# Kernel optimization log

Measured on AMD Instinct MI355X. Metric: run time of the kernel, lower is better.

## Reference

```python
import jax, jax.numpy as jnp
import numpy as np

B, S, D = 8, 4096, 64

def setup_inputs() -> dict:
    key = jax.random.key(0)
    k1, k2 = jax.random.split(key)
    x = jax.random.normal(k1, (B, S, D), dtype=jnp.float32)
    y = jax.random.normal(k2, (B, S, D), dtype=jnp.float32)
    return {"x": x, "y": y}

def reference(x, y):
    # Unscaled bidirectional cross-attention.
    # m1: [B, Sx, Sy] = x @ y^T ; m2: [B, Sy, Sx] = y @ x^T (= m1^T, but keep faithful form)
    m1 = jnp.einsum('bsd,btd->bst', x, y)
    m2 = jnp.einsum('btd,bsd->bts', y, x)
    n1 = jax.nn.softmax(m1, axis=-1)
    n2 = jax.nn.softmax(m2, axis=-1)
    o1 = jnp.einsum('bst,btd->bsd', n1, y)
    o2 = jnp.einsum('bts,bsd->btd', n2, x)
    a1 = o1 * x
    a2 = o2 * y
    return jnp.concatenate((a1, a2), axis=-1)  # [B, S, 2D]
```

## Files before the change

kernel.cpp:

```cpp
#include <hip/hip_runtime.h>
#include <stdint.h>
#include <stddef.h>

#define SS 4096
#define DD 64
#define TK 64
#define LOG2E 1.4426950408889634f
#define NEG_M_L2 (-57.70780163555854f)

typedef short    short4v __attribute__((ext_vector_type(4)));
typedef short    short8 __attribute__((ext_vector_type(8)));
typedef _Float16 half8  __attribute__((ext_vector_type(8)));
typedef float    f32x4  __attribute__((ext_vector_type(4)));
typedef __bf16   bf16x8 __attribute__((ext_vector_type(8)));

typedef __attribute__((address_space(1))) void void_g;
typedef __attribute__((address_space(3))) void void_l;

static __device__ __forceinline__ unsigned short bf16_rtn(float f) {
    uint32_t u = __builtin_bit_cast(uint32_t, f);
    u += 0x7FFFu + ((u >> 16) & 1u);
    return (unsigned short)(u >> 16);
}
static __device__ __forceinline__ void gl_lds16(const void* g, void* l) {
    __builtin_amdgcn_global_load_lds((void_g*)(g), (void_l*)(l), 16, 0, 0);
}

#define MFMA_F16(A, B, C) __builtin_amdgcn_mfma_f32_16x16x32_f16( \
    __builtin_bit_cast(half8, A), __builtin_bit_cast(half8, B), (C), 0, 0, 0)
#define MFMA_BF16(A, B, C) __builtin_amdgcn_mfma_f32_16x16x32_bf16( \
    __builtin_bit_cast(bf16x8, A), __builtin_bit_cast(bf16x8, B), (C), 0, 0, 0)

__global__ __launch_bounds__(256) void prep(
    const float* __restrict__ x, const float* __restrict__ y,
    _Float16* __restrict__ fx, _Float16* __restrict__ fy,
    unsigned short* __restrict__ tx, unsigned short* __restrict__ ty) {
    __shared__ float tile[64 * 69];
    int bid = blockIdx.x;
    int mat = bid >> 9;
    int rem = bid & 511;
    int b = rem >> 6, t64 = rem & 63;
    int s0 = t64 * 64;
    const float* src = (mat ? y : x) + ((size_t)b * SS + s0) * 64;
    _Float16* fr = (mat ? fy : fx) + ((size_t)b * SS + s0) * 64;
    unsigned short* tr = (mat ? ty : tx) + (size_t)b * SS * 64;
    int tid = threadIdx.x;
#pragma unroll
    for (int it = 0; it < 4; ++it) {
        int qi = it * 256 + tid;
        int r = qi >> 4, c4 = (qi & 15) * 4;
        f32x4 v = *(const f32x4*)(src + r * 64 + c4);
#pragma unroll
        for (int j = 0; j < 4; ++j) tile[r * 69 + c4 + j] = v[j];
    }
    __syncthreads();
#pragma unroll
    for (int j2 = 0; j2 < 2; ++j2) {
        int seg = j2 * 256 + tid;
        int r = seg >> 3, g = seg & 7;
        half8 h;
#pragma unroll
        for (int j = 0; j < 8; ++j) h[j] = (_Float16)tile[r * 69 + g * 8 + j];
        *(half8*)(fr + (size_t)r * 64 + ((g + r) & 7) * 8) = h;
    }
#pragma unroll
    for (int j2 = 0; j2 < 2; ++j2) {
        int seg = j2 * 256 + tid;
        int d = seg >> 3, k8 = seg & 7;
        short8 h;
#pragma unroll
        for (int i = 0; i < 8; ++i)
            h[i] = (short)bf16_rtn(tile[(k8 * 8 + i) * 69 + d]);
        *(short8*)(tr + (size_t)d * SS + s0 + ((k8 + d) & 7) * 8) = h;
    }
}

__global__ __launch_bounds__(256, 4)
void biattn(const float* __restrict__ xg, const float* __restrict__ yg,
            const _Float16* __restrict__ fx, const _Float16* __restrict__ fy,
            const unsigned short* __restrict__ tx, const unsigned short* __restrict__ ty,
            float* __restrict__ wsO, float* __restrict__ wsL,
            float* __restrict__ out, int mode) {
    __shared__ _Float16 shK[TK * DD];
    __shared__ unsigned short shVt[DD * TK];
    __shared__ unsigned short shP[4][32][40];

    const int bid = blockIdx.x;
    const int g8 = bid >> 3;
    int half, bd, qb;
    qb = g8 & 31;
    if (mode) { half = (g8 >> 5) & 1; bd = (bid & 7) + 8 * (g8 >> 6); }
    else      { half = 0;             bd = (bid & 7) + 8 * (g8 >> 5); }
    const int b = bd >> 1, dir = bd & 1;
    const size_t mo = (size_t)b * SS * DD;
    const _Float16* Kf = (dir ? fx : fy) + mo;
    const unsigned short* Vt = (dir ? tx : ty) + mo;
    const _Float16* Qf = (dir ? fy : fx) + mo;
    const float* Qm = (dir ? yg : xg) + mo;

    const int tid = threadIdx.x, w = tid >> 6, ln = tid & 63;
    const int l15 = ln & 15, quad = ln >> 4;
    const int q0 = qb * 128 + w * 32;

    half8 qf[2][2];
#pragma unroll
    for (int qs = 0; qs < 2; ++qs) {
        int qrow = q0 + qs * 16 + l15;
#pragma unroll
        for (int c = 0; c < 2; ++c)
            qf[qs][c] = *(const half8*)(Qf + (size_t)qrow * 64 +
                                        ((c * 4 + quad + qrow) & 7) * 8);
    }

    f32x4 Oa[2][4], La[2];
#pragma unroll
    for (int qs = 0; qs < 2; ++qs) {
        La[qs] = (f32x4){0.f, 0.f, 0.f, 0.f};
#pragma unroll
        for (int dt = 0; dt < 4; ++dt) Oa[qs][dt] = (f32x4){0.f, 0.f, 0.f, 0.f};
    }
    short8 onesb;
#pragma unroll
    for (int j = 0; j < 8; ++j) onesb[j] = (short)0x3F80;

    const int kblo = mode ? half * (SS / 2) : 0;
    const int kbhi = mode ? kblo + (SS / 2) : SS;

    for (int kb = kblo; kb < kbhi; kb += TK) {
        __syncthreads();
#pragma unroll
        for (int i = 0; i < 4; ++i) {
            int seg = w * 4 + i;
            if (seg < 8) {
                gl_lds16(Kf + (size_t)kb * 64 + seg * 512 + ln * 8,
                         (void*)(shK + seg * 512));
            } else {
                int s2 = seg - 8;
                int d = s2 * 8 + (ln >> 3);
                gl_lds16(Vt + (size_t)d * SS + kb + (ln & 7) * 8,
                         (void*)(shVt + s2 * 512));
            }
        }
        __syncthreads();

#pragma unroll
        for (int c32 = 0; c32 < 2; ++c32) {
            const int kc = c32 * 32;
            f32x4 sacc[2][2];
#pragma unroll
            for (int qs = 0; qs < 2; ++qs)
#pragma unroll
                for (int st = 0; st < 2; ++st)
                    sacc[qs][st] = (f32x4){0.f, 0.f, 0.f, 0.f};
#pragma unroll
            for (int st = 0; st < 2; ++st) {
                const int krow = kc + st * 16 + l15;
                const _Float16* hr = shK + krow * 64;
                half8 a0 = *(const half8*)(hr + ((quad + krow) & 7) * 8);
                half8 a1 = *(const half8*)(hr + ((quad + 4 + krow) & 7) * 8);
#pragma unroll
                for (int qs = 0; qs < 2; ++qs) {
                    f32x4 acc = sacc[qs][st];
                    acc = MFMA_F16(a0, qf[qs][0], acc);
                    acc = MFMA_F16(a1, qf[qs][1], acc);
                    sacc[qs][st] = acc;
                }
            }
#pragma unroll
            for (int qs = 0; qs < 2; ++qs) {
#pragma unroll
                for (int st = 0; st < 2; ++st) {
                    f32x4 s = sacc[qs][st];
                    float p0 = __builtin_amdgcn_exp2f(__builtin_fmaf(s[0], LOG2E, NEG_M_L2));
                    float p1 = __builtin_amdgcn_exp2f(__builtin_fmaf(s[1], LOG2E, NEG_M_L2));
                    float p2 = __builtin_amdgcn_exp2f(__builtin_fmaf(s[2], LOG2E, NEG_M_L2));
                    float p3 = __builtin_amdgcn_exp2f(__builtin_fmaf(s[3], LOG2E, NEG_M_L2));
                    short4v pk;
                    pk[0] = (short)bf16_rtn(p0);
                    pk[1] = (short)bf16_rtn(p1);
                    pk[2] = (short)bf16_rtn(p2);
                    pk[3] = (short)bf16_rtn(p3);
                    *(short4v*)&shP[w][qs * 16 + l15][st * 16 + quad * 4] = pk;
                }
            }
            short8 bfr0 = *(const short8*)&shP[w][l15][quad * 8];
            short8 bfr1 = *(const short8*)&shP[w][16 + l15][quad * 8];
            const int rotv = ((c32 * 4 + quad + l15) & 7) * 8;
#pragma unroll
            for (int dt = 0; dt < 4; ++dt) {
                short8 av = *(const short8*)(shVt + (dt * 16 + l15) * 64 + rotv);
                Oa[0][dt] = MFMA_BF16(av, bfr0, Oa[0][dt]);
                Oa[1][dt] = MFMA_BF16(av, bfr1, Oa[1][dt]);
            }
            La[0] = MFMA_BF16(onesb, bfr0, La[0]);
            La[1] = MFMA_BF16(onesb, bfr1, La[1]);
        }
    }

    if (mode) {
        const int pb = half * 512 + bd * 32 + qb;
#pragma unroll
        for (int qs = 0; qs < 2; ++qs) {
            float* base = wsO + (size_t)pb * 8192 + (size_t)(w * 2 + qs) * 1024
                        + l15 * 16 + quad * 4;
#pragma unroll
            for (int dt = 0; dt < 4; ++dt)
                *(f32x4*)(base + dt * 256) = Oa[qs][dt];
            if (quad == 0)
                wsL[(size_t)pb * 128 + w * 32 + qs * 16 + l15] = La[qs][0];
        }
    } else {
#pragma unroll
        for (int qs = 0; qs < 2; ++qs) {
            float inv = 1.0f / La[qs][0];
            int qrow = q0 + qs * 16 + l15;
#pragma unroll
            for (int dt = 0; dt < 4; ++dt) {
                const float* qp = Qm + (size_t)qrow * DD + dt * 16 + quad * 4;
                f32x4 xv = *(const f32x4*)qp;
                f32x4 o = Oa[qs][dt];
                f32x4 r;
#pragma unroll
                for (int j = 0; j < 4; ++j) r[j] = o[j] * inv * xv[j];
                float* op = out + ((size_t)(b * SS + qrow)) * 128 + dir * 64
                          + dt * 16 + quad * 4;
                *(f32x4*)op = r;
            }
        }
    }
}

__global__ __launch_bounds__(256) void combine(
    const float* __restrict__ xg, const float* __restrict__ yg,
    const float* __restrict__ wsO, const float* __restrict__ wsL,
    float* __restrict__ out) {
    __shared__ float t[8 * 1088];
    int pb = blockIdx.x;
    int bd = pb >> 5, qb = pb & 31;
    int b = bd >> 1, dir = bd & 1;
    const float* p0 = wsO + (size_t)pb * 8192;
    const float* p1 = wsO + (size_t)(512 + pb) * 8192;
    const float* l0 = wsL + (size_t)pb * 128;
    const float* l1 = wsL + (size_t)(512 + pb) * 128;
    const float* Qm = (dir ? yg : xg) + (size_t)b * SS * DD;
    int tid = threadIdx.x;
#pragma unroll
    for (int j = 0; j < 8; ++j) {
        int idx = j * 1024 + tid * 4;
        f32x4 a = *(const f32x4*)(p0 + idx);
        f32x4 c = *(const f32x4*)(p1 + idx);
        int dt = (idx >> 8) & 3, q = (idx >> 4) & 15, dq = idx & 15;
#pragma unroll
        for (int jj = 0; jj < 4; ++jj)
            t[j * 1088 + (dt * 16 + dq + jj) * 17 + q] = a[jj] + c[jj];
    }
    __syncthreads();
    int w2 = tid >> 6, ln = tid & 63;
    int q00 = qb * 128;
#pragma unroll 4
    for (int i = 0; i < 32; ++i) {
        int q128 = w2 * 32 + i;
        int seg = q128 >> 4, lq = q128 & 15;
        float o = t[seg * 1088 + ln * 17 + lq];
        float l = l0[q128] + l1[q128];
        float qv = Qm[(size_t)(q00 + q128) * 64 + ln];
        out[((size_t)(b * SS + q00 + q128)) * 128 + dir * 64 + ln]
            = o * (1.0f / l) * qv;
    }
}

extern "C" void kernel_launch(void* const* d_in, const int* in_sizes, int n_in,
                              void* d_out, int out_size, void* d_ws, size_t ws_size,
                              hipStream_t stream) {
    const float* x = (const float*)d_in[0];
    const float* y = (const float*)d_in[1];
    char* ws = (char*)d_ws;
    const size_t MATB = (size_t)8 * SS * DD * 2;
    _Float16* fx = (_Float16*)(ws);
    _Float16* fy = (_Float16*)(ws + MATB);
    unsigned short* tx = (unsigned short*)(ws + 2 * MATB);
    unsigned short* ty = (unsigned short*)(ws + 3 * MATB);
    float* wsO = (float*)(ws + 4 * MATB);
    float* wsL = (float*)(ws + 4 * MATB + (size_t)1024 * 8192 * 4);
    const size_t need = 4 * MATB + (size_t)1024 * 8192 * 4 + (size_t)1024 * 128 * 4;
    const int mode = (ws_size >= need) ? 1 : 0;
    (void)in_sizes; (void)n_in; (void)out_size;
    prep<<<dim3(1024), dim3(256), 0, stream>>>(x, y, fx, fy, tx, ty);
    biattn<<<dim3(mode ? 1024 : 512), dim3(256), 0, stream>>>(
        x, y, fx, fy, tx, ty, wsO, wsL, (float*)d_out, mode);
    if (mode)
        combine<<<dim3(512), dim3(256), 0, stream>>>(x, y, wsO, wsL, (float*)d_out);
}
```

Baseline: 171.3 us.

## Generalize split-K to four parts, fold log2e into Q, use packed bf16 converts

The key range is now split into up to four parts instead of two when the workspace is large enough, which multiplies the block count and needs more partial sums in combine. The log2(e) scale is folded into Q during prep, and the constant offset is used as the MFMA accumulator's initial value, so the per-element FMA before exp2 is dropped. Probability and transpose packing use a hardware packed bf16 convert when the builtin exists. The occupancy hint is raised from 4 to 6 blocks per SM, which may add register pressure.

New measurement: 496.5 us. 190% more time.

```diff
diff --git a/kernel.cpp b/kernel.cpp
--- a/kernel.cpp
+++ b/kernel.cpp
@@ -13,6 +13,8 @@
 typedef _Float16 half8  __attribute__((ext_vector_type(8)));
 typedef float    f32x4  __attribute__((ext_vector_type(4)));
 typedef __bf16   bf16x8 __attribute__((ext_vector_type(8)));
+typedef uint32_t u32x2  __attribute__((ext_vector_type(2)));
+typedef uint32_t u32x4  __attribute__((ext_vector_type(4)));
 
 typedef __attribute__((address_space(1))) void void_g;
 typedef __attribute__((address_space(3))) void void_l;
@@ -22,6 +24,17 @@
     u += 0x7FFFu + ((u >> 16) & 1u);
     return (unsigned short)(u >> 16);
 }
+#if __has_builtin(__builtin_amdgcn_cvt_pk_bf16_f32)
+typedef __bf16 bf16x2 __attribute__((ext_vector_type(2)));
+static __device__ __forceinline__ uint32_t pkbf(float a, float b) {
+    bf16x2 v = __builtin_amdgcn_cvt_pk_bf16_f32(a, b);
+    return __builtin_bit_cast(uint32_t, v);
+}
+#else
+static __device__ __forceinline__ uint32_t pkbf(float a, float b) {
+    return (uint32_t)bf16_rtn(a) | ((uint32_t)bf16_rtn(b) << 16);
+}
+#endif
 static __device__ __forceinline__ void gl_lds16(const void* g, void* l) {
     __builtin_amdgcn_global_load_lds((void_g*)(g), (void_l*)(l), 16, 0, 0);
 }
@@ -44,6 +57,7 @@
     const float* src = (mat ? y : x) + ((size_t)b * SS + s0) * 64;
     _Float16* fr = (mat ? fy : fx) + ((size_t)b * SS + s0) * 64;
     unsigned short* tr = (mat ? ty : tx) + (size_t)b * SS * 64;
+    const float sc = mat ? 1.0f : LOG2E;
     int tid = threadIdx.x;
 #pragma unroll
     for (int it = 0; it < 4; ++it) {
@@ -60,37 +74,40 @@
         int r = seg >> 3, g = seg & 7;
         half8 h;
 #pragma unroll
-        for (int j = 0; j < 8; ++j) h[j] = (_Float16)tile[r * 69 + g * 8 + j];
+        for (int j = 0; j < 8; ++j)
+            h[j] = (_Float16)(tile[r * 69 + g * 8 + j] * sc);
         *(half8*)(fr + (size_t)r * 64 + ((g + r) & 7) * 8) = h;
     }
 #pragma unroll
     for (int j2 = 0; j2 < 2; ++j2) {
         int seg = j2 * 256 + tid;
         int d = seg >> 3, k8 = seg & 7;
-        short8 h;
-#pragma unroll
-        for (int i = 0; i < 8; ++i)
-            h[i] = (short)bf16_rtn(tile[(k8 * 8 + i) * 69 + d]);
-        *(short8*)(tr + (size_t)d * SS + s0 + ((k8 + d) & 7) * 8) = h;
-    }
-}
-
-__global__ __launch_bounds__(256, 4)
+        float v[8];
+#pragma unroll
+        for (int i = 0; i < 8; ++i) v[i] = tile[(k8 * 8 + i) * 69 + d];
+        u32x4 o;
+        o[0] = pkbf(v[0], v[1]); o[1] = pkbf(v[2], v[3]);
+        o[2] = pkbf(v[4], v[5]); o[3] = pkbf(v[6], v[7]);
+        *(u32x4*)(tr + (size_t)d * SS + s0 + ((k8 + d) & 7) * 8) = o;
+    }
+}
+
+__global__ __launch_bounds__(256, 6)
 void biattn(const float* __restrict__ xg, const float* __restrict__ yg,
             const _Float16* __restrict__ fx, const _Float16* __restrict__ fy,
             const unsigned short* __restrict__ tx, const unsigned short* __restrict__ ty,
             float* __restrict__ wsO, float* __restrict__ wsL,
-            float* __restrict__ out, int mode) {
+            float* __restrict__ out, int nsplit) {
     __shared__ _Float16 shK[TK * DD];
     __shared__ unsigned short shVt[DD * TK];
     __shared__ unsigned short shP[4][32][40];
 
     const int bid = blockIdx.x;
     const int g8 = bid >> 3;
-    int half, bd, qb;
-    qb = g8 & 31;
-    if (mode) { half = (g8 >> 5) & 1; bd = (bid & 7) + 8 * (g8 >> 6); }
-    else      { half = 0;             bd = (bid & 7) + 8 * (g8 >> 5); }
+    const int qb = g8 & 31;
+    const int r2 = g8 >> 5;
+    const int bd = (bid & 7) + 8 * (r2 & 1);
+    const int part = r2 >> 1;
     const int b = bd >> 1, dir = bd & 1;
     const size_t mo = (size_t)b * SS * DD;
     const _Float16* Kf = (dir ? fx : fy) + mo;
@@ -123,8 +140,9 @@
 #pragma unroll
     for (int j = 0; j < 8; ++j) onesb[j] = (short)0x3F80;
 
-    const int kblo = mode ? half * (SS / 2) : 0;
-    const int kbhi = mode ? kblo + (SS / 2) : SS;
+    const int span = SS / nsplit;
+    const int kblo = part * span;
+    const int kbhi = kblo + span;
 
     for (int kb = kblo; kb < kbhi; kb += TK) {
         __syncthreads();
@@ -151,7 +169,7 @@
             for (int qs = 0; qs < 2; ++qs)
 #pragma unroll
                 for (int st = 0; st < 2; ++st)
-                    sacc[qs][st] = (f32x4){0.f, 0.f, 0.f, 0.f};
+                    sacc[qs][st] = (f32x4){NEG_M_L2, NEG_M_L2, NEG_M_L2, NEG_M_L2};
 #pragma unroll
             for (int st = 0; st < 2; ++st) {
                 const int krow = kc + st * 16 + l15;
@@ -168,20 +186,21 @@
             }
 #pragma unroll
             for (int qs = 0; qs < 2; ++qs) {
-#pragma unroll
-                for (int st = 0; st < 2; ++st) {
-                    f32x4 s = sacc[qs][st];
-                    float p0 = __builtin_amdgcn_exp2f(__builtin_fmaf(s[0], LOG2E, NEG_M_L2));
-                    float p1 = __builtin_amdgcn_exp2f(__builtin_fmaf(s[1], LOG2E, NEG_M_L2));
-                    float p2 = __builtin_amdgcn_exp2f(__builtin_fmaf(s[2], LOG2E, NEG_M_L2));
-                    float p3 = __builtin_amdgcn_exp2f(__builtin_fmaf(s[3], LOG2E, NEG_M_L2));
-                    short4v pk;
-                    pk[0] = (short)bf16_rtn(p0);
-                    pk[1] = (short)bf16_rtn(p1);
-                    pk[2] = (short)bf16_rtn(p2);
-                    pk[3] = (short)bf16_rtn(p3);
-                    *(short4v*)&shP[w][qs * 16 + l15][st * 16 + quad * 4] = pk;
-                }
+                f32x4 s0 = sacc[qs][0], s1 = sacc[qs][1];
+                float p0 = __builtin_amdgcn_exp2f(s0[0]);
+                float p1 = __builtin_amdgcn_exp2f(s0[1]);
+                float p2 = __builtin_amdgcn_exp2f(s0[2]);
+                float p3 = __builtin_amdgcn_exp2f(s0[3]);
+                float p4 = __builtin_amdgcn_exp2f(s1[0]);
+                float p5 = __builtin_amdgcn_exp2f(s1[1]);
+                float p6 = __builtin_amdgcn_exp2f(s1[2]);
+                float p7 = __builtin_amdgcn_exp2f(s1[3]);
+                u32x2 w0, w1;
+                w0[0] = pkbf(p0, p1); w0[1] = pkbf(p2, p3);
+                w1[0] = pkbf(p4, p5); w1[1] = pkbf(p6, p7);
+                unsigned short* pr = &shP[w][qs * 16 + l15][0];
+                *(u32x2*)(pr + quad * 4)      = w0;
+                *(u32x2*)(pr + 16 + quad * 4) = w1;
             }
             short8 bfr0 = *(const short8*)&shP[w][l15][quad * 8];
             short8 bfr1 = *(const short8*)&shP[w][16 + l15][quad * 8];
@@ -197,8 +216,8 @@
         }
     }
 
-    if (mode) {
-        const int pb = half * 512 + bd * 32 + qb;
+    if (nsplit > 1) {
+        const int pb = part * 512 + bd * 32 + qb;
 #pragma unroll
         for (int qs = 0; qs < 2; ++qs) {
             float* base = wsO + (size_t)pb * 8192 + (size_t)(w * 2 + qs) * 1024
@@ -233,26 +252,26 @@
 __global__ __launch_bounds__(256) void combine(
     const float* __restrict__ xg, const float* __restrict__ yg,
     const float* __restrict__ wsO, const float* __restrict__ wsL,
-    float* __restrict__ out) {
+    float* __restrict__ out, int nsplit) {
     __shared__ float t[8 * 1088];
     int pb = blockIdx.x;
     int bd = pb >> 5, qb = pb & 31;
     int b = bd >> 1, dir = bd & 1;
-    const float* p0 = wsO + (size_t)pb * 8192;
-    const float* p1 = wsO + (size_t)(512 + pb) * 8192;
-    const float* l0 = wsL + (size_t)pb * 128;
-    const float* l1 = wsL + (size_t)(512 + pb) * 128;
     const float* Qm = (dir ? yg : xg) + (size_t)b * SS * DD;
     int tid = threadIdx.x;
 #pragma unroll
     for (int j = 0; j < 8; ++j) {
         int idx = j * 1024 + tid * 4;
-        f32x4 a = *(const f32x4*)(p0 + idx);
-        f32x4 c = *(const f32x4*)(p1 + idx);
+        f32x4 a = {0.f, 0.f, 0.f, 0.f};
+        for (int s = 0; s < nsplit; ++s) {
+            f32x4 v = *(const f32x4*)(wsO + (size_t)(s * 512 + pb) * 8192 + idx);
+#pragma unroll
+            for (int jj = 0; jj < 4; ++jj) a[jj] += v[jj];
+        }
         int dt = (idx >> 8) & 3, q = (idx >> 4) & 15, dq = idx & 15;
 #pragma unroll
         for (int jj = 0; jj < 4; ++jj)
-            t[j * 1088 + (dt * 16 + dq + jj) * 17 + q] = a[jj] + c[jj];
+            t[j * 1088 + (dt * 16 + dq + jj) * 17 + q] = a[jj];
     }
     __syncthreads();
     int w2 = tid >> 6, ln = tid & 63;
@@ -262,7 +281,9 @@
         int q128 = w2 * 32 + i;
         int seg = q128 >> 4, lq = q128 & 15;
         float o = t[seg * 1088 + ln * 17 + lq];
-        float l = l0[q128] + l1[q128];
+        float l = 0.f;
+        for (int s = 0; s < nsplit; ++s)
+            l += wsL[(size_t)(s * 512 + pb) * 128 + q128];
         float qv = Qm[(size_t)(q00 + q128) * 64 + ln];
         out[((size_t)(b * SS + q00 + q128)) * 128 + dir * 64 + ln]
             = o * (1.0f / l) * qv;
@@ -280,14 +301,18 @@
     _Float16* fy = (_Float16*)(ws + MATB);
     unsigned short* tx = (unsigned short*)(ws + 2 * MATB);
     unsigned short* ty = (unsigned short*)(ws + 3 * MATB);
+    const size_t PBB = (size_t)512 * 8192 * 4;
+    const size_t LBB = (size_t)512 * 128 * 4;
+    int nsplit = 1;
+    if (ws_size >= 4 * MATB + 4 * (PBB + LBB)) nsplit = 4;
+    else if (ws_size >= 4 * MATB + 2 * (PBB + LBB)) nsplit = 2;
     float* wsO = (float*)(ws + 4 * MATB);
-    float* wsL = (float*)(ws + 4 * MATB + (size_t)1024 * 8192 * 4);
-    const size_t need = 4 * MATB + (size_t)1024 * 8192 * 4 + (size_t)1024 * 128 * 4;
-    const int mode = (ws_size >= need) ? 1 : 0;
+    float* wsL = (float*)(ws + 4 * MATB + (size_t)nsplit * PBB);
     (void)in_sizes; (void)n_in; (void)out_size;
     prep<<<dim3(1024), dim3(256), 0, stream>>>(x, y, fx, fy, tx, ty);
-    biattn<<<dim3(mode ? 1024 : 512), dim3(256), 0, stream>>>(
-        x, y, fx, fy, tx, ty, wsO, wsL, (float*)d_out, mode);
-    if (mode)
-        combine<<<dim3(512), dim3(256), 0, stream>>>(x, y, wsO, wsL, (float*)d_out);
-}
+    biattn<<<dim3(512 * nsplit), dim3(256), 0, stream>>>(
+        x, y, fx, fy, tx, ty, wsO, wsL, (float*)d_out, nsplit);
+    if (nsplit > 1)
+        combine<<<dim3(512), dim3(256), 0, stream>>>(x, y, wsO, wsL,
+                                                     (float*)d_out, nsplit);
+}
```
